# Performance work log

Hardware: AMD Instinct MI355X
Metric: run time of the kernel (lower is better)

Reference implementation:

```python
import jax, jax.numpy as jnp
import numpy as np

N, D, B = 50000, 256, 2048
SIGMA = 1.0
SIGMA2 = SIGMA * SIGMA  # module stores np.square(sigma)


def setup_inputs() -> dict:
    key = jax.random.key(0)
    k1, k2, k3, k4 = jax.random.split(key, 4)
    x = jax.random.normal(k1, (B, D), dtype=jnp.float32)
    data_set = jax.random.normal(k2, (N, D), dtype=jnp.float32)
    # labels are +/-1
    data_labels = jnp.where(jax.random.uniform(k3, (N,)) < 0.5, -1.0, 1.0).astype(jnp.float32)
    # lambdas initialized to ones in the module; use small positive noise around 1/n scale
    lambdas = jax.random.uniform(k4, (N,), dtype=jnp.float32) * (2.0 / N)
    b = jnp.ones((1,), dtype=jnp.float32)
    return {"x": x, "data_set": data_set, "data_labels": data_labels,
            "lambdas": lambdas, "b": b}


def reference(x, data_set, data_labels, lambdas, b):
    x2 = jnp.sum(x * x, axis=1, keepdims=True)            # [B,1]
    s2 = jnp.sum(data_set * data_set, axis=1)             # [N]
    cross = jnp.einsum('bd,nd->bn', x, data_set)          # [B,N]
    sqdist = x2 + s2[None, :] - 2.0 * cross               # [B,N]
    K = jnp.exp(-sqdist / (2.0 * SIGMA2))                 # rbf kernel [B,N]
    w = data_labels * jax.nn.relu(lambdas)                # [N]
    return jnp.tanh(K @ w + b)                            # [B]
```

## Files before the change

kernel.cpp:

```cpp
#include <hip/hip_runtime.h>
#include <hip/hip_bf16.h>
#include <math.h>

#define NPTS 50000
#define DIM  256
#define BQ   2048
#define NPAD 50048

#define BK   32
#define CH   32
#define NCH32 1564
#define NG   64
#define LOG2E 1.4426950408889634f

#define WS_ACC 0
#define WS_X2  2048
#define WS_T   4096
#define WS_SGN 54144
#define WS_XB  104192
#define WS_SB  366336
#define WS_TOTAL_BYTES (6772480ull * 4ull)

#define V1_ACC 0
#define V1_X2  2048
#define V1_S2  4096
#define V1_W   54096

typedef __bf16 bf16x8 __attribute__((ext_vector_type(8)));
typedef __bf16 bf16x4 __attribute__((ext_vector_type(4)));
typedef float  f32x4  __attribute__((ext_vector_type(4)));
typedef unsigned int u32;

__device__ __forceinline__ float fast_exp2(float v) {
#if __has_builtin(__builtin_amdgcn_exp2f)
  return __builtin_amdgcn_exp2f(v);
#else
  return exp2f(v);
#endif
}

__device__ __forceinline__ void async_copy16(const __bf16* g, __bf16* l) {
  __builtin_amdgcn_global_load_lds(
      (const __attribute__((address_space(1))) u32*)g,
      (__attribute__((address_space(3))) u32*)l, 16, 0, 0);
}


__global__ __launch_bounds__(256) void svm_precvt9(
    const float* __restrict__ x, const float* __restrict__ s,
    const float* __restrict__ labels, const float* __restrict__ lambdas,
    float* __restrict__ ws) {
  const int wid  = blockIdx.x * 4 + (threadIdx.x >> 6);
  const int lane = threadIdx.x & 63;
  __bf16* xb = (__bf16*)(ws + WS_XB);
  __bf16* sb = (__bf16*)(ws + WS_SB);

  if (blockIdx.x < 8) ws[WS_ACC + blockIdx.x * 256 + threadIdx.x] = 0.0f;

  if (wid < NPAD) {
    float4 v = make_float4(0.f, 0.f, 0.f, 0.f);
    if (wid < NPTS)
      v = reinterpret_cast<const float4*>(s + (size_t)wid * DIM)[lane];
    bf16x4 h = { (__bf16)v.x, (__bf16)v.y, (__bf16)v.z, (__bf16)v.w };
    *reinterpret_cast<bf16x4*>(sb + (size_t)wid * DIM + lane * 4) = h;
    float ss = v.x * v.x + v.y * v.y + v.z * v.z + v.w * v.w;
    #pragma unroll
    for (int off = 32; off > 0; off >>= 1) ss += __shfl_xor(ss, off);
    if (lane == 0) {
      float s2h = 0.5f * LOG2E * ss;
      float lam = (wid < NPTS) ? lambdas[wid] : 0.0f;
      float lab = (wid < NPTS) ? labels[wid] : 1.0f;
      float mag = lam > 0.0f ? lam : 0.0f;
      ws[WS_T + wid]   = (mag > 0.0f) ? s2h - log2f(mag) : __builtin_inff();
      ws[WS_SGN + wid] = lab;
    }
  } else if (wid < NPAD + BQ) {
    int r = wid - NPAD;
    float4 v = reinterpret_cast<const float4*>(x + (size_t)r * DIM)[lane];
    bf16x4 h = { (__bf16)v.x, (__bf16)v.y, (__bf16)v.z, (__bf16)v.w };
    *reinterpret_cast<bf16x4*>(xb + (size_t)r * DIM + lane * 4) = h;
    float ss = v.x * v.x + v.y * v.y + v.z * v.z + v.w * v.w;
    #pragma unroll
    for (int off = 32; off > 0; off >>= 1) ss += __shfl_xor(ss, off);
    if (lane == 0) ws[WS_X2 + r] = 0.5f * LOG2E * ss;
  }
}

__global__ __launch_bounds__(256, 2) void svm_main19(float* __restrict__ ws) {
  __shared__ __bf16 sB[3][8 * CH * 32];

  const __bf16* xb = (const __bf16*)(ws + WS_XB);
  const __bf16* sb = (const __bf16*)(ws + WS_SB);
  const float* x2g = ws + WS_X2;
  const float* tg  = ws + WS_T;
  const float* sgg = ws + WS_SGN;
  float* accOut    = ws + WS_ACC;

  const int t    = threadIdx.x;
  const int wave = t >> 6;
  const int lane = t & 63;
  const int quad = lane >> 4;
  const int l16  = lane & 15;
  const int g    = blockIdx.x & (NG - 1);
  const int mt   = blockIdx.x >> 6;
  const int m0   = mt * 256;
  const int c0   = (NCH32 * g) / NG;
  const int c1   = (NCH32 * (g + 1)) / NG;

  const int srcswz = ((lane & 3) ^ ((lane >> 3) & 3)) * 8;
  const int rdswz = (quad ^ ((l16 >> 1) & 3)) * 8;

#define STAGE19(buf, cc)                                                      \
  do {                                                                        \
    _Pragma("unroll")                                                         \
    for (int i = 0; i < 4; ++i) {                                             \
      int chn = wave * 4 + i;                                      \
      int kt = chn >> 1;                                           \
      int nb = (chn & 1) * 16;                                     \
      const __bf16* src = sb + (size_t)((cc) * CH + nb + (lane >> 2)) * DIM   \
                             + kt * BK + srcswz;                              \
      async_copy16(src, &sB[(buf)][kt * (CH * 32) + nb * 32] + lane * 8);     \
    }                                                                         \
  } while (0)

  STAGE19(0, c0);
  STAGE19(1, c0 + 1);

  f32x4 afr[4][8];
  #pragma unroll
  for (int mi = 0; mi < 4; ++mi)
    #pragma unroll
    for (int kt = 0; kt < 8; ++kt)
      afr[mi][kt] = *reinterpret_cast<const f32x4*>(
          xb + (size_t)(m0 + wave * 64 + mi * 16 + l16) * DIM + kt * BK + quad * 8);
  #pragma unroll
  for (int mi = 0; mi < 4; ++mi)
    #pragma unroll
    for (int kt = 0; kt < 8; ++kt)
      asm volatile("" : "+v"(afr[mi][kt]));

  float runAcc[4][4] = {{0.f, 0.f, 0.f, 0.f}, {0.f, 0.f, 0.f, 0.f},
                        {0.f, 0.f, 0.f, 0.f}, {0.f, 0.f, 0.f, 0.f}};

  asm volatile("s_waitcnt vmcnt(4)" ::: "memory");
  __builtin_amdgcn_s_barrier();

  int cur = 0;
  for (int c = c0; c < c1; ++c) {
    float tt[2], sg[2];
    #pragma unroll
    for (int ni = 0; ni < 2; ++ni) {
      int n = c * CH + ni * 16 + l16;
      tt[ni] = tg[n];
      sg[ni] = sgg[n];
    }
    __builtin_amdgcn_sched_barrier(0);

    {
      int c2 = c + 2;
      if (c2 < c1) {
        int b2 = cur + 2; if (b2 >= 3) b2 -= 3;
        STAGE19(b2, c2);
      }
    }

    f32x4 acc[4][2];
    #pragma unroll
    for (int mi = 0; mi < 4; ++mi)
      #pragma unroll
      for (int ni = 0; ni < 2; ++ni)
        acc[mi][ni] = (f32x4)(0.0f);

    const __bf16* bufB = &sB[cur][0];
    #pragma unroll
    for (int kt = 0; kt < 8; ++kt) {
      bf16x8 bfv[2];
      #pragma unroll
      for (int ni = 0; ni < 2; ++ni)
        bfv[ni] = *reinterpret_cast<const bf16x8*>(
            bufB + kt * (CH * 32) + (ni * 16 + l16) * 32 + rdswz);
      #pragma unroll
      for (int mi = 0; mi < 4; ++mi)
        #pragma unroll
        for (int ni = 0; ni < 2; ++ni)
          acc[mi][ni] = __builtin_amdgcn_mfma_f32_16x16x32_bf16(
              __builtin_bit_cast(bf16x8, afr[mi][kt]), bfv[ni],
              acc[mi][ni], 0, 0, 0);
    }

    #pragma unroll
    for (int mi = 0; mi < 4; ++mi)
      #pragma unroll
      for (int reg = 0; reg < 4; ++reg) {
        float p = runAcc[mi][reg];
        #pragma unroll
        for (int ni = 0; ni < 2; ++ni)
          p = __builtin_fmaf(sg[ni],
                fast_exp2(__builtin_fmaf(acc[mi][ni][reg], LOG2E, -tt[ni])), p);
        runAcc[mi][reg] = p;
      }

    __builtin_amdgcn_s_barrier();
    asm volatile("" ::: "memory");
    cur = (cur + 1 < 3) ? cur + 1 : 0;
  }

  #pragma unroll
  for (int mi = 0; mi < 4; ++mi)
    #pragma unroll
    for (int reg = 0; reg < 4; ++reg) {
      float v = runAcc[mi][reg];
      v += __shfl_xor(v, 1);
      v += __shfl_xor(v, 2);
      v += __shfl_xor(v, 4);
      v += __shfl_xor(v, 8);
      if (l16 == 0) {
        int row = m0 + wave * 64 + mi * 16 + quad * 4 + reg;
        atomicAdd(&accOut[row], fast_exp2(-x2g[row]) * v);
      }
    }
#undef STAGE19
}


__global__ __launch_bounds__(256) void svm_precompute(
    const float* __restrict__ x, const float* __restrict__ s,
    const float* __restrict__ labels, const float* __restrict__ lambdas,
    float* __restrict__ ws) {
  int wid  = blockIdx.x * 4 + (threadIdx.x >> 6);
  int lane = threadIdx.x & 63;
  const float* src;
  if (wid < NPTS)           src = s + (size_t)wid * DIM;
  else if (wid < NPTS + BQ) src = x + (size_t)(wid - NPTS) * DIM;
  else return;
  float4 v = reinterpret_cast<const float4*>(src)[lane];
  float ss = v.x * v.x + v.y * v.y + v.z * v.z + v.w * v.w;
  #pragma unroll
  for (int off = 32; off > 0; off >>= 1) ss += __shfl_xor(ss, off);
  if (lane == 0) {
    if (wid < NPTS) {
      ws[V1_S2 + wid] = ss;
      float lam = lambdas[wid];
      ws[V1_W + wid] = labels[wid] * (lam > 0.0f ? lam : 0.0f);
    } else {
      ws[V1_X2 + (wid - NPTS)] = ss;
    }
  }
}

__global__ __launch_bounds__(256) void svm_main(
    const float* __restrict__ x, const float* __restrict__ s,
    const float* __restrict__ ws) {
  __shared__ __bf16 sA[128 * BK];
  __shared__ __bf16 sB2[128 * BK];

  const int t    = threadIdx.x;
  const int wave = t >> 6;
  const int lane = t & 63;
  const int quad = lane >> 4;
  const int l16  = lane & 15;
  const int wm   = (wave & 1) * 64;
  const int wn   = (wave >> 1) * 64;
  const int bRow0 = blockIdx.y * 128;
  const int n0    = blockIdx.x * 128;

  f32x4 acc[4][4];
  #pragma unroll
  for (int i = 0; i < 4; ++i)
    #pragma unroll
    for (int j = 0; j < 4; ++j)
      acc[i][j] = (f32x4)(0.0f);

  for (int kt = 0; kt < DIM / BK; ++kt) {
    const int k0 = kt * BK;
    __syncthreads();
    #pragma unroll
    for (int i = 0; i < 4; ++i) {
      int slot = t + i * 256;
      int r  = slot >> 3;
      int c4 = slot & 7;
      float4 va = reinterpret_cast<const float4*>(
          x + (size_t)(bRow0 + r) * DIM + k0)[c4];
      bf16x4 ha = { (__bf16)va.x, (__bf16)va.y, (__bf16)va.z, (__bf16)va.w };
      *reinterpret_cast<bf16x4*>(&sA[r * BK + c4 * 4]) = ha;

      int nrow = n0 + r;
      float4 vb = make_float4(0.f, 0.f, 0.f, 0.f);
      if (nrow < NPTS)
        vb = reinterpret_cast<const float4*>(
            s + (size_t)nrow * DIM + k0)[c4];
      bf16x4 hb = { (__bf16)vb.x, (__bf16)vb.y, (__bf16)vb.z, (__bf16)vb.w };
      *reinterpret_cast<bf16x4*>(&sB2[r * BK + c4 * 4]) = hb;
    }
    __syncthreads();

    bf16x8 af[4], bfv[4];
    #pragma unroll
    for (int mi = 0; mi < 4; ++mi)
      af[mi] = *reinterpret_cast<const bf16x8*>(
          &sA[(wm + mi * 16 + l16) * BK + quad * 8]);
    #pragma unroll
    for (int ni = 0; ni < 4; ++ni)
      bfv[ni] = *reinterpret_cast<const bf16x8*>(
          &sB2[(wn + ni * 16 + l16) * BK + quad * 8]);
    #pragma unroll
    for (int mi = 0; mi < 4; ++mi)
      #pragma unroll
      for (int ni = 0; ni < 4; ++ni)
        acc[mi][ni] = __builtin_amdgcn_mfma_f32_16x16x32_bf16(
            af[mi], bfv[ni], acc[mi][ni], 0, 0, 0);
  }

  const float* x2g = ws + V1_X2;
  const float* s2g = ws + V1_S2;
  const float* wg  = ws + V1_W;
  float* accOut    = (float*)ws + V1_ACC;

  float s2v[4], wv[4];
  #pragma unroll
  for (int ni = 0; ni < 4; ++ni) {
    int n = n0 + wn + ni * 16 + l16;
    bool ok = n < NPTS;
    s2v[ni] = ok ? s2g[n] : 0.0f;
    wv[ni]  = ok ? wg[n]  : 0.0f;
  }
  #pragma unroll
  for (int mi = 0; mi < 4; ++mi) {
    const int mbase = wm + mi * 16 + quad * 4;
    #pragma unroll
    for (int reg = 0; reg < 4; ++reg) {
      float x2r = x2g[bRow0 + mbase + reg];
      float ps = 0.0f;
      #pragma unroll
      for (int ni = 0; ni < 4; ++ni) {
        float cc = acc[mi][ni][reg];
        ps += __expf(__builtin_fmaf(-0.5f, x2r + s2v[ni], cc)) * wv[ni];
      }
      ps += __shfl_xor(ps, 1);
      ps += __shfl_xor(ps, 2);
      ps += __shfl_xor(ps, 4);
      ps += __shfl_xor(ps, 8);
      if (l16 == 0) atomicAdd(&accOut[bRow0 + mbase + reg], ps);
    }
  }
}


__global__ __launch_bounds__(256) void svm_finalize(
    const float* __restrict__ ws, const float* __restrict__ bias,
    float* __restrict__ out) {
  int i = blockIdx.x * 256 + threadIdx.x;
  if (i < BQ) out[i] = tanhf(ws[i] + bias[0]);
}

extern "C" void kernel_launch(void* const* d_in, const int* in_sizes, int n_in,
                              void* d_out, int out_size, void* d_ws, size_t ws_size,
                              hipStream_t stream) {
  const float* x       = (const float*)d_in[0];
  const float* s       = (const float*)d_in[1];
  const float* labels  = (const float*)d_in[2];
  const float* lambdas = (const float*)d_in[3];
  const float* bias    = (const float*)d_in[4];
  float* out = (float*)d_out;
  float* ws  = (float*)d_ws;

  if (ws_size >= WS_TOTAL_BYTES) {
    svm_precvt9<<<(NPAD + BQ + 3) / 4, 256, 0, stream>>>(x, s, labels, lambdas, ws);
    svm_main19<<<8 * NG, 256, 0, stream>>>(ws);
  } else {
    hipMemsetAsync(ws, 0, BQ * sizeof(float), stream);
    svm_precompute<<<(NPTS + BQ + 3) / 4, 256, 0, stream>>>(x, s, labels, lambdas, ws);
    dim3 grid(391, BQ / 128);
    svm_main<<<grid, 256, 0, stream>>>(x, s, ws);
  }
  svm_finalize<<<BQ / 256, 256, 0, stream>>>(ws, bias, out);
}
```

Before: 154.0 us.

## Switch distance GEMM from bf16 to fp8 e4m3 with 32x32x64 scaled MFMA

The precompute kernel now converts x and the data set to fp8 e4m3 instead of bf16. The main kernel uses the gfx950 scaled MFMA 32x32x64 f8f6f4 instruction with unit scales, and its LDS staging, swizzle, fragment layout and epilogue reduction are rewritten for the new tile shape. This halves the bytes moved and doubles MFMA throughput. The cost is a large loss of precision in the dot products, which then feed exp(), so accuracy may fall outside tolerance.

```diff
diff --git a/kernel.cpp b/kernel.cpp
--- a/kernel.cpp
+++ b/kernel.cpp
@@ -1,5 +1,6 @@
 #include <hip/hip_runtime.h>
 #include <hip/hip_bf16.h>
+#include <hip/hip_fp8.h>
 #include <math.h>
 
 #define NPTS 50000
@@ -7,7 +8,6 @@
 #define BQ   2048
 #define NPAD 50048
 
-#define BK   32
 #define CH   32
 #define NCH32 1564
 #define NG   64
@@ -29,7 +29,11 @@
 typedef __bf16 bf16x8 __attribute__((ext_vector_type(8)));
 typedef __bf16 bf16x4 __attribute__((ext_vector_type(4)));
 typedef float  f32x4  __attribute__((ext_vector_type(4)));
+typedef float  f32x16 __attribute__((ext_vector_type(16)));
+typedef int    i32x4  __attribute__((ext_vector_type(4)));
+typedef int    i32x8  __attribute__((ext_vector_type(8)));
 typedef unsigned int u32;
+typedef unsigned char u8;
 
 __device__ __forceinline__ float fast_exp2(float v) {
 #if __has_builtin(__builtin_amdgcn_exp2f)
@@ -39,21 +43,32 @@
 #endif
 }
 
-__device__ __forceinline__ void async_copy16(const __bf16* g, __bf16* l) {
+__device__ __forceinline__ void async_copy16(const void* g, void* l) {
   __builtin_amdgcn_global_load_lds(
       (const __attribute__((address_space(1))) u32*)g,
       (__attribute__((address_space(3))) u32*)l, 16, 0, 0);
 }
 
-
-__global__ __launch_bounds__(256) void svm_precvt9(
+__device__ __forceinline__ u32 pack_fp8x4(float4 v) {
+#if __has_builtin(__builtin_amdgcn_cvt_pk_fp8_f32)
+  int pk = __builtin_amdgcn_cvt_pk_fp8_f32(v.x, v.y, 0, false);
+  pk = __builtin_amdgcn_cvt_pk_fp8_f32(v.z, v.w, pk, true);
+  return (u32)pk;
+#else
+  __hip_fp8_e4m3 a(v.x), b(v.y), c(v.z), d(v.w);
+  return (u32)a.__x | ((u32)b.__x << 8) | ((u32)c.__x << 16) | ((u32)d.__x << 24);
+#endif
+}
+
+
+__global__ __launch_bounds__(256) void svm_precvt10(
     const float* __restrict__ x, const float* __restrict__ s,
     const float* __restrict__ labels, const float* __restrict__ lambdas,
     float* __restrict__ ws) {
   const int wid  = blockIdx.x * 4 + (threadIdx.x >> 6);
   const int lane = threadIdx.x & 63;
-  __bf16* xb = (__bf16*)(ws + WS_XB);
-  __bf16* sb = (__bf16*)(ws + WS_SB);
+  u8* xb8 = (u8*)(ws + WS_XB);
+  u8* sb8 = (u8*)(ws + WS_SB);
 
   if (blockIdx.x < 8) ws[WS_ACC + blockIdx.x * 256 + threadIdx.x] = 0.0f;
 
@@ -61,8 +76,7 @@
     float4 v = make_float4(0.f, 0.f, 0.f, 0.f);
     if (wid < NPTS)
       v = reinterpret_cast<const float4*>(s + (size_t)wid * DIM)[lane];
-    bf16x4 h = { (__bf16)v.x, (__bf16)v.y, (__bf16)v.z, (__bf16)v.w };
-    *reinterpret_cast<bf16x4*>(sb + (size_t)wid * DIM + lane * 4) = h;
+    ((u32*)(sb8 + (size_t)wid * DIM))[lane] = pack_fp8x4(v);
     float ss = v.x * v.x + v.y * v.y + v.z * v.z + v.w * v.w;
     #pragma unroll
     for (int off = 32; off > 0; off >>= 1) ss += __shfl_xor(ss, off);
@@ -77,8 +91,7 @@
   } else if (wid < NPAD + BQ) {
     int r = wid - NPAD;
     float4 v = reinterpret_cast<const float4*>(x + (size_t)r * DIM)[lane];
-    bf16x4 h = { (__bf16)v.x, (__bf16)v.y, (__bf16)v.z, (__bf16)v.w };
-    *reinterpret_cast<bf16x4*>(xb + (size_t)r * DIM + lane * 4) = h;
+    ((u32*)(xb8 + (size_t)r * DIM))[lane] = pack_fp8x4(v);
     float ss = v.x * v.x + v.y * v.y + v.z * v.z + v.w * v.w;
     #pragma unroll
     for (int off = 32; off > 0; off >>= 1) ss += __shfl_xor(ss, off);
@@ -86,11 +99,11 @@
   }
 }
 
-__global__ __launch_bounds__(256, 2) void svm_main19(float* __restrict__ ws) {
-  __shared__ __bf16 sB[3][8 * CH * 32];
-
-  const __bf16* xb = (const __bf16*)(ws + WS_XB);
-  const __bf16* sb = (const __bf16*)(ws + WS_SB);
+__global__ __launch_bounds__(256, 2) void svm_main20(float* __restrict__ ws) {
+  __shared__ u8 sB[3][8192];
+
+  const u8* xb8 = (const u8*)(ws + WS_XB);
+  const u8* sb8 = (const u8*)(ws + WS_SB);
   const float* x2g = ws + WS_X2;
   const float* tg  = ws + WS_T;
   const float* sgg = ws + WS_SGN;
@@ -99,106 +112,92 @@
   const int t    = threadIdx.x;
   const int wave = t >> 6;
   const int lane = t & 63;
-  const int quad = lane >> 4;
-  const int l16  = lane & 15;
+  const int l32  = lane & 31;
+  const int hk   = lane >> 5;
   const int g    = blockIdx.x & (NG - 1);
   const int mt   = blockIdx.x >> 6;
   const int m0   = mt * 256;
   const int c0   = (NCH32 * g) / NG;
   const int c1   = (NCH32 * (g + 1)) / NG;
 
-  const int srcswz = ((lane & 3) ^ ((lane >> 3) & 3)) * 8;
-  const int rdswz = (quad ^ ((l16 >> 1) & 3)) * 8;
-
-#define STAGE19(buf, cc)                                                      \
+#define STAGE20(buf, cc)                                                      \
   do {                                                                        \
     _Pragma("unroll")                                                         \
-    for (int i = 0; i < 4; ++i) {                                             \
-      int chn = wave * 4 + i;                                      \
-      int kt = chn >> 1;                                           \
-      int nb = (chn & 1) * 16;                                     \
-      const __bf16* src = sb + (size_t)((cc) * CH + nb + (lane >> 2)) * DIM   \
-                             + kt * BK + srcswz;                              \
-      async_copy16(src, &sB[(buf)][kt * (CH * 32) + nb * 32] + lane * 8);     \
+    for (int i = 0; i < 2; ++i) {                                             \
+      int p  = wave * 2 + i;                                        \
+      int kt = p >> 1;                                              \
+      int h  = p & 1;                                                         \
+      int r  = h * 16 + (lane >> 2);                                          \
+      int q  = (lane & 3) ^ ((r >> 1) & 3);                                   \
+      const u8* src = sb8 + (size_t)((cc) * CH + r) * DIM + kt * 64 + q * 16; \
+      async_copy16(src, &sB[(buf)][kt * 2048 + h * 1024 + lane * 16]);        \
     }                                                                         \
   } while (0)
 
-  STAGE19(0, c0);
-  STAGE19(1, c0 + 1);
-
-  f32x4 afr[4][8];
-  #pragma unroll
-  for (int mi = 0; mi < 4; ++mi)
-    #pragma unroll
-    for (int kt = 0; kt < 8; ++kt)
-      afr[mi][kt] = *reinterpret_cast<const f32x4*>(
-          xb + (size_t)(m0 + wave * 64 + mi * 16 + l16) * DIM + kt * BK + quad * 8);
-  #pragma unroll
-  for (int mi = 0; mi < 4; ++mi)
-    #pragma unroll
-    for (int kt = 0; kt < 8; ++kt)
+  STAGE20(0, c0);
+  STAGE20(1, c0 + 1);
+
+  i32x8 afr[2][4];
+  #pragma unroll
+  for (int mi = 0; mi < 2; ++mi)
+    #pragma unroll
+    for (int kt = 0; kt < 4; ++kt) {
+      const u8* ap = xb8 + (size_t)(m0 + wave * 64 + mi * 32 + l32) * DIM
+                         + kt * 64 + hk * 32;
+      i32x4 a0 = *reinterpret_cast<const i32x4*>(ap);
+      i32x4 a1 = *reinterpret_cast<const i32x4*>(ap + 16);
+      afr[mi][kt] = __builtin_shufflevector(a0, a1, 0, 1, 2, 3, 4, 5, 6, 7);
+    }
+  #pragma unroll
+  for (int mi = 0; mi < 2; ++mi)
+    #pragma unroll
+    for (int kt = 0; kt < 4; ++kt)
       asm volatile("" : "+v"(afr[mi][kt]));
 
-  float runAcc[4][4] = {{0.f, 0.f, 0.f, 0.f}, {0.f, 0.f, 0.f, 0.f},
-                        {0.f, 0.f, 0.f, 0.f}, {0.f, 0.f, 0.f, 0.f}};
-
-  asm volatile("s_waitcnt vmcnt(4)" ::: "memory");
+  float runAcc0[16], runAcc1[16];
+  #pragma unroll
+  for (int i = 0; i < 16; ++i) { runAcc0[i] = 0.0f; runAcc1[i] = 0.0f; }
+
+  asm volatile("s_waitcnt vmcnt(2)" ::: "memory");
   __builtin_amdgcn_s_barrier();
 
   int cur = 0;
   for (int c = c0; c < c1; ++c) {
-    float tt[2], sg[2];
-    #pragma unroll
-    for (int ni = 0; ni < 2; ++ni) {
-      int n = c * CH + ni * 16 + l16;
-      tt[ni] = tg[n];
-      sg[ni] = sgg[n];
-    }
+    float tt = tg[c * CH + l32];
+    float sg = sgg[c * CH + l32];
     __builtin_amdgcn_sched_barrier(0);
 
     {
       int c2 = c + 2;
       if (c2 < c1) {
         int b2 = cur + 2; if (b2 >= 3) b2 -= 3;
-        STAGE19(b2, c2);
+        STAGE20(b2, c2);
       }
     }
 
-    f32x4 acc[4][2];
-    #pragma unroll
-    for (int mi = 0; mi < 4; ++mi)
-      #pragma unroll
-      for (int ni = 0; ni < 2; ++ni)
-        acc[mi][ni] = (f32x4)(0.0f);
-
-    const __bf16* bufB = &sB[cur][0];
-    #pragma unroll
-    for (int kt = 0; kt < 8; ++kt) {
-      bf16x8 bfv[2];
-      #pragma unroll
-      for (int ni = 0; ni < 2; ++ni)
-        bfv[ni] = *reinterpret_cast<const bf16x8*>(
-            bufB + kt * (CH * 32) + (ni * 16 + l16) * 32 + rdswz);
-      #pragma unroll
-      for (int mi = 0; mi < 4; ++mi)
-        #pragma unroll
-        for (int ni = 0; ni < 2; ++ni)
-          acc[mi][ni] = __builtin_amdgcn_mfma_f32_16x16x32_bf16(
-              __builtin_bit_cast(bf16x8, afr[mi][kt]), bfv[ni],
-              acc[mi][ni], 0, 0, 0);
-    }
-
-    #pragma unroll
-    for (int mi = 0; mi < 4; ++mi)
-      #pragma unroll
-      for (int reg = 0; reg < 4; ++reg) {
-        float p = runAcc[mi][reg];
-        #pragma unroll
-        for (int ni = 0; ni < 2; ++ni)
-          p = __builtin_fmaf(sg[ni],
-                fast_exp2(__builtin_fmaf(acc[mi][ni][reg], LOG2E, -tt[ni])), p);
-        runAcc[mi][reg] = p;
-      }
+    f32x16 acc0 = (f32x16)(0.0f), acc1 = (f32x16)(0.0f);
+    const u8* bufB = &sB[cur][0];
+    #pragma unroll
+    for (int kt = 0; kt < 4; ++kt) {
+      int s0 = ((l32 << 2) | (hk << 1)) ^ ((l32 >> 1) & 3);
+      const u8* bp = bufB + kt * 2048;
+      i32x4 lo = *reinterpret_cast<const i32x4*>(bp + s0 * 16);
+      i32x4 hi = *reinterpret_cast<const i32x4*>(bp + (s0 ^ 1) * 16);
+      i32x8 bfr = __builtin_shufflevector(lo, hi, 0, 1, 2, 3, 4, 5, 6, 7);
+      acc0 = __builtin_amdgcn_mfma_scale_f32_32x32x64_f8f6f4(
+          afr[0][kt], bfr, acc0, 0, 0, 0, 0x7F7F7F7F, 0, 0x7F7F7F7F);
+      acc1 = __builtin_amdgcn_mfma_scale_f32_32x32x64_f8f6f4(
+          afr[1][kt], bfr, acc1, 0, 0, 0, 0x7F7F7F7F, 0, 0x7F7F7F7F);
+    }
+
+    #pragma unroll
+    for (int reg = 0; reg < 16; ++reg)
+      runAcc0[reg] = __builtin_fmaf(
+          sg, fast_exp2(__builtin_fmaf(acc0[reg], LOG2E, -tt)), runAcc0[reg]);
+    #pragma unroll
+    for (int reg = 0; reg < 16; ++reg)
+      runAcc1[reg] = __builtin_fmaf(
+          sg, fast_exp2(__builtin_fmaf(acc1[reg], LOG2E, -tt)), runAcc1[reg]);
 
     __builtin_amdgcn_s_barrier();
     asm volatile("" ::: "memory");
@@ -206,22 +205,36 @@
   }
 
   #pragma unroll
-  for (int mi = 0; mi < 4; ++mi)
-    #pragma unroll
-    for (int reg = 0; reg < 4; ++reg) {
-      float v = runAcc[mi][reg];
-      v += __shfl_xor(v, 1);
-      v += __shfl_xor(v, 2);
-      v += __shfl_xor(v, 4);
-      v += __shfl_xor(v, 8);
-      if (l16 == 0) {
-        int row = m0 + wave * 64 + mi * 16 + quad * 4 + reg;
-        atomicAdd(&accOut[row], fast_exp2(-x2g[row]) * v);
-      }
-    }
-#undef STAGE19
-}
-
+  for (int reg = 0; reg < 16; ++reg) {
+    float v = runAcc0[reg];
+    v += __shfl_xor(v, 1);
+    v += __shfl_xor(v, 2);
+    v += __shfl_xor(v, 4);
+    v += __shfl_xor(v, 8);
+    v += __shfl_xor(v, 16);
+    if (l32 == 0) {
+      int row = m0 + wave * 64 + (reg & 3) + 8 * (reg >> 2) + 4 * hk;
+      atomicAdd(&accOut[row], fast_exp2(-x2g[row]) * v);
+    }
+  }
+  #pragma unroll
+  for (int reg = 0; reg < 16; ++reg) {
+    float v = runAcc1[reg];
+    v += __shfl_xor(v, 1);
+    v += __shfl_xor(v, 2);
+    v += __shfl_xor(v, 4);
+    v += __shfl_xor(v, 8);
+    v += __shfl_xor(v, 16);
+    if (l32 == 0) {
+      int row = m0 + wave * 64 + 32 + (reg & 3) + 8 * (reg >> 2) + 4 * hk;
+      atomicAdd(&accOut[row], fast_exp2(-x2g[row]) * v);
+    }
+  }
+#undef STAGE20
+}
+
+
+#define BK 32
 
 __global__ __launch_bounds__(256) void svm_precompute(
     const float* __restrict__ x, const float* __restrict__ s,
@@ -365,8 +378,8 @@
   float* ws  = (float*)d_ws;
 
   if (ws_size >= WS_TOTAL_BYTES) {
-    svm_precvt9<<<(NPAD + BQ + 3) / 4, 256, 0, stream>>>(x, s, labels, lambdas, ws);
-    svm_main19<<<8 * NG, 256, 0, stream>>>(ws);
+    svm_precvt10<<<(NPAD + BQ + 3) / 4, 256, 0, stream>>>(x, s, labels, lambdas, ws);
+    svm_main20<<<8 * NG, 256, 0, stream>>>(ws);
   } else {
     hipMemsetAsync(ws, 0, BQ * sizeof(float), stream);
     svm_precompute<<<(NPTS + BQ + 3) / 4, 256, 0, stream>>>(x, s, labels, lambdas, ws);
```

New measurement: 144.9 us. 1.06x faster.
